# Performance work log

Measured on AMD Instinct MI355X. Metric: run time of the kernel, lower is better.

Reference implementation:

```python
import jax, jax.numpy as jnp
import numpy as np

MAXDISP = 320
NEG_SLOPE = 0.2


def _lrelu(x):
    return jnp.where(x >= 0, x, NEG_SLOPE * x)


def _conv(x, w, b, stride):
    # NCHW conv, VALID padding (torch Conv2d with padding=0)
    y = jax.lax.conv_general_dilated(x, w, window_strides=stride, padding='VALID',
                                     dimension_numbers=('NCHW', 'OIHW', 'NCHW'))
    return y + b[None, :, None, None]


def _tile_pair(fl, fr, wa, ba, wb, bb):
    # left: 4x4 conv stride (4,4); right: ZeroPad2d((0,3,0,0)) then stride (4,1)
    tl = _lrelu(_conv(_lrelu(_conv(fl, wa, ba, (4, 4))), wb, bb, (1, 1)))
    frp = jnp.pad(fr, ((0, 0), (0, 0), (0, 0), (0, 3)))
    tr = _lrelu(_conv(_lrelu(_conv(frp, wa, ba, (4, 1))), wb, bb, (1, 1)))
    return tl, tr


def _calc_init_disp(fl, fr, D):
    # fl: [B,C,h,w4], fr: [B,C,h,w] with w = 4*w4.
    # grid_sample(nearest, align_corners=True) with integer coords reduces to
    # exact gather at right column index 4*j - d, zero outside (padding_mode=zeros).
    B, C, h, w4 = fl.shape
    w = fr.shape[3]
    j = jnp.arange(w4)
    d = jnp.arange(D)
    idx = 4 * j[None, :] - d[:, None]              # [D, w4]
    valid = idx >= 0                               # only left edge can go OOB
    idxc = jnp.clip(idx, 0, w - 1)
    fr_g = fr[:, :, :, idxc]                       # [B,C,h,D,w4]
    fr_g = jnp.where(valid[None, None, None, :, :], fr_g, jnp.zeros((), fr.dtype))
    cv = jnp.abs(fl[:, :, :, None, :] - fr_g).sum(axis=1)  # L1 over C -> [B,h,D,w4]
    return jnp.transpose(cv, (0, 2, 1, 3))         # [B,D,h,w4]


def _level_hyp(cv, dscrpt_feat, dw, db):
    min_cost = jnp.min(cv, axis=1, keepdims=True)
    disp = jnp.argmin(cv, axis=1, keepdims=True).astype(cv.dtype)
    dscrpt = _lrelu(_conv(jnp.concatenate([min_cost, dscrpt_feat], axis=1), dw, db, (1, 1)))
    z = jnp.zeros_like(disp)
    return jnp.concatenate([disp, z, z, dscrpt], axis=1)  # [B,16,h,w]


def setup_inputs() -> dict:
    key = jax.random.key(0)
    ks = iter(jax.random.split(key, 64))

    def rn(shape, s=1.0):
        return jax.random.normal(next(ks), shape, dtype=jnp.float32) * s

    B, H, W = 1, 384, 1280
    inp = {
        'fea_l16': rn((B, 32, H // 16, W // 16)), 'fea_l8': rn((B, 24, H // 8, W // 8)),
        'fea_l4': rn((B, 24, H // 4, W // 4)), 'fea_l2': rn((B, 16, H // 2, W // 2)),
        'fea_l1': rn((B, 16, H, W)),
        'fea_r16': rn((B, 32, H // 16, W // 16)), 'fea_r8': rn((B, 24, H // 8, W // 8)),
        'fea_r4': rn((B, 24, H // 4, W // 4)), 'fea_r2': rn((B, 16, H // 2, W // 2)),
        'fea_r1': rn((B, 16, H, W)),
    }
    fea_c = {16: 32, 8: 24, 4: 24, 2: 16, 1: 16}
    for s, c in fea_c.items():
        inp[f'tcw{s}a'] = rn((16, c, 4, 4), 0.1)
        inp[f'tcb{s}a'] = rn((16,), 0.1)
        inp[f'tcw{s}b'] = rn((16, 16, 1, 1), 0.1)
        inp[f'tcb{s}b'] = rn((16,), 0.1)
    dsc_in = {16: 17, 8: 17, 4: 33, 2: 25, 1: 25}
    for s, c in dsc_in.items():
        inp[f'dw{s}'] = rn((13, c, 1, 1), 0.1)
        inp[f'db{s}'] = rn((13,), 0.1)
    return inp


def reference(fea_l16, fea_l8, fea_l4, fea_l2, fea_l1,
              fea_r16, fea_r8, fea_r4, fea_r2, fea_r1,
              tcw16a, tcb16a, tcw16b, tcb16b,
              tcw8a, tcb8a, tcw8b, tcb8b,
              tcw4a, tcb4a, tcw4b, tcb4b,
              tcw2a, tcb2a, tcw2b, tcb2b,
              tcw1a, tcb1a, tcw1b, tcb1b,
              dw16, db16, dw8, db8, dw4, db4, dw2, db2, dw1, db1):
    tl16, tr16 = _tile_pair(fea_l16, fea_r16, tcw16a, tcb16a, tcw16b, tcb16b)
    tl8, tr8 = _tile_pair(fea_l8, fea_r8, tcw8a, tcb8a, tcw8b, tcb8b)
    tl4, tr4 = _tile_pair(fea_l4, fea_r4, tcw4a, tcb4a, tcw4b, tcb4b)
    tl2, tr2 = _tile_pair(fea_l2, fea_r2, tcw2a, tcb2a, tcw2b, tcb2b)
    tl1, tr1 = _tile_pair(fea_l1, fea_r1, tcw1a, tcb1a, tcw1b, tcb1b)

    cv16 = _calc_init_disp(tl16, tr16, MAXDISP // 16)
    cv8 = _calc_init_disp(tl8, tr8, MAXDISP // 8)
    cv4 = _calc_init_disp(tl4, tr4, MAXDISP // 4)
    cv2 = _calc_init_disp(tl2, tr2, MAXDISP // 2)
    cv1 = _calc_init_disp(tl1, tr1, MAXDISP)

    hyp16 = _level_hyp(cv16, tl16, dw16, db16)
    hyp8 = _level_hyp(cv8, tl8, dw8, db8)
    hyp4 = _level_hyp(cv4, fea_l16, dw4, db4)
    hyp2 = _level_hyp(cv2, fea_l8, dw2, db2)
    hyp1 = _level_hyp(cv1, fea_l4, dw1, db1)

    return (cv16, cv8, cv4, cv2, cv1, hyp16, hyp8, hyp4, hyp2, hyp1)
```

## Files before the change

kernel.cpp:

```cpp
#include <hip/hip_runtime.h>
#include <float.h>

#define NEG_SLOPE 0.2f

__device__ __forceinline__ float lrelu(float x) { return x >= 0.0f ? x : NEG_SLOPE * x; }

struct PrepSeg { const float* wa; const float* wb; float* wat; float* wbt; int CIN; };
struct PrepTab { PrepSeg seg[5]; };

__global__ __launch_bounds__(256)
void prep_weights(PrepTab tab) {
    PrepSeg sg = tab.seg[blockIdx.x];
    int n = sg.CIN * 256;
    for (int i = threadIdx.x; i < n; i += 256)
        sg.wat[i] = sg.wa[(i & 15) * (sg.CIN * 16) + (i >> 4)];
    sg.wbt[threadIdx.x] = sg.wb[(threadIdx.x & 15) * 16 + (threadIdx.x >> 4)];
}

struct ConvSeg {
    const float* in; const float* wat; const float* wbt; const float* ba; const float* bb;
    float* out;
    int CIN, H, W, SX, OW, npix, blk0;
};
struct ConvTab { ConvSeg seg[10]; };

__global__ __launch_bounds__(256)
void conv_uber(ConvTab tab) {
    int si = 0;
#pragma unroll
    for (int i = 1; i < 10; i++) if ((int)blockIdx.x >= tab.seg[i].blk0) si = i;
    const ConvSeg sg = tab.seg[si];

    int pix = ((int)blockIdx.x - sg.blk0) * 256 + threadIdx.x;
    const bool valid = pix < sg.npix;
    int cpix = valid ? pix : sg.npix - 1;
    int y = cpix / sg.OW, x = cpix - y * sg.OW;

    float m[16];
#pragma unroll
    for (int co = 0; co < 16; co++) m[co] = 0.f;

    const int W = sg.W, H = sg.H, CIN = sg.CIN;
    const int xb = (sg.SX == 4) ? 4 * x : x;
    const bool fast = (sg.SX == 4) || (x + 4 <= W);
    const float* ib = sg.in + (size_t)(4 * y) * W;

    if (fast) {
        for (int c = 0; c < CIN; c++) {
            const float* rb = ib + (size_t)c * H * W + xb;
            const float* wc = sg.wat + c * 256;
#pragma unroll
            for (int r = 0; r < 4; r++) {
                float4 v = *(const float4*)(rb + r * W);
                const float* wr = wc + r * 64;
#pragma unroll
                for (int co = 0; co < 16; co++) m[co] = fmaf(v.x, wr[co], m[co]);
#pragma unroll
                for (int co = 0; co < 16; co++) m[co] = fmaf(v.y, wr[16 + co], m[co]);
#pragma unroll
                for (int co = 0; co < 16; co++) m[co] = fmaf(v.z, wr[32 + co], m[co]);
#pragma unroll
                for (int co = 0; co < 16; co++) m[co] = fmaf(v.w, wr[48 + co], m[co]);
            }
        }
    } else {
        for (int c = 0; c < CIN; c++) {
            const float* rb = ib + (size_t)c * H * W;
            const float* wc = sg.wat + c * 256;
#pragma unroll
            for (int r = 0; r < 4; r++) {
                const float* wr = wc + r * 64;
#pragma unroll
                for (int kx = 0; kx < 4; kx++) {
                    int col = xb + kx;
                    float v = (col < W) ? rb[r * W + col] : 0.f;
                    const float* w2 = wr + kx * 16;
#pragma unroll
                    for (int co = 0; co < 16; co++) m[co] = fmaf(v, w2[co], m[co]);
                }
            }
        }
    }

#pragma unroll
    for (int co = 0; co < 16; co++) m[co] = lrelu(m[co] + sg.ba[co]);

    float o[16];
#pragma unroll
    for (int co = 0; co < 16; co++) o[co] = 0.f;
#pragma unroll
    for (int k = 0; k < 16; k++) {
        float mk = m[k];
        const float* wr = sg.wbt + k * 16;
#pragma unroll
        for (int co = 0; co < 16; co++) o[co] = fmaf(mk, wr[co], o[co]);
    }
    if (valid) {
#pragma unroll
        for (int co = 0; co < 16; co++)
            sg.out[(size_t)co * sg.npix + pix] = lrelu(o[co] + sg.bb[co]);
    }
}

struct CvSeg {
    const float* tl; const float* tr; const float* feat;
    const float* dw; const float* db;
    float* cv; float* hyp;
    int h, w4, w, D, gpc, CF, blk0;
};
struct CvTab { CvSeg seg[5]; };

__global__ __launch_bounds__(256)
void cv_hyp_uber(CvTab tab) {
    __shared__ float smin[256];
    __shared__ int sarg[256];

    int si = 0;
#pragma unroll
    for (int i = 1; i < 5; i++) if ((int)blockIdx.x >= tab.seg[i].blk0) si = i;
    const CvSeg sg = tab.seg[si];

    const int npix = sg.h * sg.w4;
    const int p = threadIdx.x & 63, chunk = threadIdx.x >> 6;
    const int pix = ((int)blockIdx.x - sg.blk0) * 64 + p;
    const bool valid = pix < npix;

    float mloc = FLT_MAX; int aloc = 0;
    if (valid) {
        int y = pix / sg.w4, j = pix - y * sg.w4;
        float tlv[16]; float sumabs = 0.f;
#pragma unroll
        for (int c = 0; c < 16; c++) { tlv[c] = sg.tl[(size_t)c * npix + pix]; sumabs += fabsf(tlv[c]); }

        int ngroups = sg.D >> 2;
        int g0 = chunk * sg.gpc;
        int g1 = min(ngroups, g0 + sg.gpc);
        const float* trrow = sg.tr + (size_t)y * sg.w;
        int hw = sg.h * sg.w;

        float carry[16];
        int b0 = 4 * j - 4 * g0;
        if (g0 < g1 && b0 >= 0) {
#pragma unroll
            for (int c = 0; c < 16; c++) carry[c] = trrow[(size_t)c * hw + b0];
        }
        for (int g = g0; g < g1; g++) {
            int b = 4 * j - 4 * g;
            float a0, a1, a2, a3;
            if (b >= 4) {
                a0 = a1 = a2 = a3 = 0.f;
#pragma unroll
                for (int c = 0; c < 16; c++) {
                    float4 f0 = *(const float4*)(trrow + (size_t)c * hw + (b - 4));
                    float tv = tlv[c];
                    a0 += fabsf(tv - carry[c]);
                    a1 += fabsf(tv - f0.w);
                    a2 += fabsf(tv - f0.z);
                    a3 += fabsf(tv - f0.y);
                    carry[c] = f0.x;
                }
            } else if (b == 0) {
                a0 = 0.f; a1 = a2 = a3 = sumabs;
#pragma unroll
                for (int c = 0; c < 16; c++) a0 += fabsf(tlv[c] - carry[c]);
            } else {
                a0 = a1 = a2 = a3 = sumabs;
            }
            float* cvp = sg.cv + (size_t)(4 * g) * npix + pix;
            cvp[0] = a0; cvp[npix] = a1; cvp[2 * (size_t)npix] = a2; cvp[3 * (size_t)npix] = a3;
            if (a0 < mloc) { mloc = a0; aloc = 4 * g; }
            if (a1 < mloc) { mloc = a1; aloc = 4 * g + 1; }
            if (a2 < mloc) { mloc = a2; aloc = 4 * g + 2; }
            if (a3 < mloc) { mloc = a3; aloc = 4 * g + 3; }
        }
    }
    smin[threadIdx.x] = mloc;
    sarg[threadIdx.x] = aloc;
    __syncthreads();

    if (threadIdx.x < 64 && valid) {
        float mn = smin[threadIdx.x]; int arg = sarg[threadIdx.x];
#pragma unroll
        for (int c2 = 1; c2 < 4; c2++) {
            float v = smin[c2 * 64 + threadIdx.x];
            if (v < mn) { mn = v; arg = sarg[c2 * 64 + threadIdx.x]; }
        }
        float acc[13];
#pragma unroll
        for (int o = 0; o < 13; o++) acc[o] = sg.dw[o * (sg.CF + 1)] * mn;
        for (int c = 0; c < sg.CF; c++) {
            float v = sg.feat[(size_t)c * npix + pix];
#pragma unroll
            for (int o = 0; o < 13; o++) acc[o] = fmaf(v, sg.dw[o * (sg.CF + 1) + 1 + c], acc[o]);
        }
        sg.hyp[pix] = (float)arg;
        sg.hyp[npix + pix] = 0.f;
        sg.hyp[2 * (size_t)npix + pix] = 0.f;
#pragma unroll
        for (int o = 0; o < 13; o++) sg.hyp[(size_t)(3 + o) * npix + pix] = lrelu(acc[o] + sg.db[o]);
    }
}

extern "C" void kernel_launch(void* const* d_in, const int* in_sizes, int n_in,
                              void* d_out, int out_size, void* d_ws, size_t ws_size,
                              hipStream_t stream) {
    (void)in_sizes; (void)n_in; (void)out_size; (void)ws_size;
    float* out = (float*)d_out;
    float* ws = (float*)d_ws;

    const int C[5] = {32, 24, 24, 16, 16};
    const int H[5] = {24, 48, 96, 192, 384};
    const int W[5] = {80, 160, 320, 640, 1280};
    const int D[5] = {20, 40, 80, 160, 320};
    const int wa_i[5] = {10, 14, 18, 22, 26};
    const int dw_i[5] = {30, 32, 34, 36, 38};

    const size_t cv_off[5]  = {0, 2400, 21600, 175200, 1404000};
    const size_t hyp_off[5] = {11234400, 11236320, 11244000, 11274720, 11397600};
    const size_t tl_off[5] = {0, 9600, 48000, 201600, 816000};
    const size_t tr_off[5] = {1920, 17280, 78720, 324480, 1307520};
    const size_t wat_off[5] = {3280000, 3288192, 3294336, 3300480, 3304576};
    const size_t wbt_off[5] = {3310000, 3310256, 3310512, 3310768, 3311024};

    const float* fl[5] = {(const float*)d_in[0], (const float*)d_in[1], (const float*)d_in[2],
                          (const float*)d_in[3], (const float*)d_in[4]};
    const float* fr[5] = {(const float*)d_in[5], (const float*)d_in[6], (const float*)d_in[7],
                          (const float*)d_in[8], (const float*)d_in[9]};

    PrepTab pt;
    for (int l = 0; l < 5; l++) {
        pt.seg[l].wa = (const float*)d_in[wa_i[l]];
        pt.seg[l].wb = (const float*)d_in[wa_i[l] + 2];
        pt.seg[l].wat = ws + wat_off[l];
        pt.seg[l].wbt = ws + wbt_off[l];
        pt.seg[l].CIN = C[l];
    }
    prep_weights<<<5, 256, 0, stream>>>(pt);

    const int ord_lvl[10]  = {4, 4, 3, 3, 2, 2, 1, 1, 0, 0};
    const int ord_side[10] = {1, 0, 1, 0, 1, 0, 1, 0, 1, 0};
    ConvTab ct;
    int blk = 0;
    for (int i = 0; i < 10; i++) {
        int l = ord_lvl[i]; bool right = ord_side[i];
        ConvSeg& s = ct.seg[i];
        s.in = right ? fr[l] : fl[l];
        s.wat = ws + wat_off[l];
        s.wbt = ws + wbt_off[l];
        s.ba = (const float*)d_in[wa_i[l] + 1];
        s.bb = (const float*)d_in[wa_i[l] + 3];
        s.out = ws + (right ? tr_off[l] : tl_off[l]);
        s.CIN = C[l]; s.H = H[l]; s.W = W[l];
        s.SX = right ? 1 : 4;
        s.OW = right ? W[l] : W[l] / 4;
        s.npix = (H[l] / 4) * s.OW;
        s.blk0 = blk;
        blk += (s.npix + 255) / 256;
    }
    conv_uber<<<blk, 256, 0, stream>>>(ct);

    const float* feat[5] = {ws + tl_off[0], ws + tl_off[1], fl[0], fl[1], fl[2]};
    const int   CF[5]    = {16, 16, 32, 24, 24};
    CvTab vt;
    blk = 0;
    for (int i = 0; i < 5; i++) {
        int l = 4 - i;
        CvSeg& s = vt.seg[i];
        s.tl = ws + tl_off[l]; s.tr = ws + tr_off[l];
        s.feat = feat[l];
        s.dw = (const float*)d_in[dw_i[l]];
        s.db = (const float*)d_in[dw_i[l] + 1];
        s.cv = out + cv_off[l]; s.hyp = out + hyp_off[l];
        s.h = H[l] / 4; s.w4 = W[l] / 4; s.w = W[l]; s.D = D[l];
        int ngroups = D[l] / 4;
        s.gpc = (ngroups + 3) / 4;
        s.CF = CF[l];
        s.blk0 = blk;
        blk += (s.h * s.w4 + 63) / 64;
    }
    cv_hyp_uber<<<blk, 256, 0, stream>>>(vt);
}
```

Baseline: 366.3 us.

## Compute four adjacent right-tile outputs per thread to reuse loaded input rows

The right-side stride-(4,1) conv now has each thread produce four consecutive output columns. It loads two float4s per row and reuses them across the overlapping 4-wide windows, then writes float4 stores. This cuts redundant global loads, launches four times fewer blocks for the right side, and amortizes weight reads across more FMAs. In exchange it raises register pressure (64 accumulators plus 64 outputs), which may lower occupancy or cause spills.

Result: slower. 736.3 us (+101.0%).

```diff
diff --git a/kernel.cpp b/kernel.cpp
--- a/kernel.cpp
+++ b/kernel.cpp
@@ -20,7 +20,7 @@
 struct ConvSeg {
     const float* in; const float* wat; const float* wbt; const float* ba; const float* bb;
     float* out;
-    int CIN, H, W, SX, OW, npix, blk0;
+    int CIN, H, W, right, nit, npix, blk0;
 };
 struct ConvTab { ConvSeg seg[10]; };
 
@@ -31,23 +31,75 @@
     for (int i = 1; i < 10; i++) if ((int)blockIdx.x >= tab.seg[i].blk0) si = i;
     const ConvSeg sg = tab.seg[si];
 
-    int pix = ((int)blockIdx.x - sg.blk0) * 256 + threadIdx.x;
-    const bool valid = pix < sg.npix;
-    int cpix = valid ? pix : sg.npix - 1;
-    int y = cpix / sg.OW, x = cpix - y * sg.OW;
-
-    float m[16];
-#pragma unroll
-    for (int co = 0; co < 16; co++) m[co] = 0.f;
-
+    int t = ((int)blockIdx.x - sg.blk0) * 256 + threadIdx.x;
+    const bool valid = t < sg.nit;
+    int ct = valid ? t : sg.nit - 1;
     const int W = sg.W, H = sg.H, CIN = sg.CIN;
-    const int xb = (sg.SX == 4) ? 4 * x : x;
-    const bool fast = (sg.SX == 4) || (x + 4 <= W);
-    const float* ib = sg.in + (size_t)(4 * y) * W;
-
-    if (fast) {
+    const int W4 = W >> 2;
+    int y = ct / W4, xq = ct - y * W4;
+    int colb = 4 * xq;
+    const float* ib = sg.in + (size_t)(4 * y) * W + colb;
+
+    if (sg.right) {
+        float m[4][16];
+#pragma unroll
+        for (int i = 0; i < 4; i++)
+#pragma unroll
+            for (int co = 0; co < 16; co++) m[i][co] = 0.f;
+
+        const bool has1 = colb + 4 < W;
         for (int c = 0; c < CIN; c++) {
-            const float* rb = ib + (size_t)c * H * W + xb;
+            const float* rb = ib + (size_t)c * H * W;
+            const float* wc = sg.wat + c * 256;
+#pragma unroll
+            for (int r = 0; r < 4; r++) {
+                float4 f0 = *(const float4*)(rb + r * W);
+                float4 f1 = make_float4(0.f, 0.f, 0.f, 0.f);
+                if (has1) f1 = *(const float4*)(rb + r * W + 4);
+                float wv[8] = {f0.x, f0.y, f0.z, f0.w, f1.x, f1.y, f1.z, f1.w};
+                const float* wr = wc + r * 64;
+#pragma unroll
+                for (int i = 0; i < 4; i++) {
+#pragma unroll
+                    for (int kx = 0; kx < 4; kx++) {
+                        float v = wv[i + kx];
+                        const float* w2 = wr + kx * 16;
+#pragma unroll
+                        for (int co = 0; co < 16; co++) m[i][co] = fmaf(v, w2[co], m[i][co]);
+                    }
+                }
+            }
+        }
+        float o[4][16];
+#pragma unroll
+        for (int i = 0; i < 4; i++) {
+#pragma unroll
+            for (int co = 0; co < 16; co++) m[i][co] = lrelu(m[i][co] + sg.ba[co]);
+#pragma unroll
+            for (int co = 0; co < 16; co++) o[i][co] = 0.f;
+#pragma unroll
+            for (int k = 0; k < 16; k++) {
+                float mk = m[i][k];
+                const float* wr = sg.wbt + k * 16;
+#pragma unroll
+                for (int co = 0; co < 16; co++) o[i][co] = fmaf(mk, wr[co], o[i][co]);
+            }
+        }
+        if (valid) {
+            size_t base = (size_t)y * W + colb;
+#pragma unroll
+            for (int co = 0; co < 16; co++) {
+                float4 v = make_float4(lrelu(o[0][co] + sg.bb[co]), lrelu(o[1][co] + sg.bb[co]),
+                                       lrelu(o[2][co] + sg.bb[co]), lrelu(o[3][co] + sg.bb[co]));
+                *(float4*)(sg.out + (size_t)co * sg.npix + base) = v;
+            }
+        }
+    } else {
+        float m[16];
+#pragma unroll
+        for (int co = 0; co < 16; co++) m[co] = 0.f;
+        for (int c = 0; c < CIN; c++) {
+            const float* rb = ib + (size_t)c * H * W;
             const float* wc = sg.wat + c * 256;
 #pragma unroll
             for (int r = 0; r < 4; r++) {
@@ -63,42 +115,23 @@
                 for (int co = 0; co < 16; co++) m[co] = fmaf(v.w, wr[48 + co], m[co]);
             }
         }
-    } else {
-        for (int c = 0; c < CIN; c++) {
-            const float* rb = ib + (size_t)c * H * W;
-            const float* wc = sg.wat + c * 256;
-#pragma unroll
-            for (int r = 0; r < 4; r++) {
-                const float* wr = wc + r * 64;
-#pragma unroll
-                for (int kx = 0; kx < 4; kx++) {
-                    int col = xb + kx;
-                    float v = (col < W) ? rb[r * W + col] : 0.f;
-                    const float* w2 = wr + kx * 16;
-#pragma unroll
-                    for (int co = 0; co < 16; co++) m[co] = fmaf(v, w2[co], m[co]);
-                }
-            }
-        }
-    }
-
-#pragma unroll
-    for (int co = 0; co < 16; co++) m[co] = lrelu(m[co] + sg.ba[co]);
-
-    float o[16];
-#pragma unroll
-    for (int co = 0; co < 16; co++) o[co] = 0.f;
-#pragma unroll
-    for (int k = 0; k < 16; k++) {
-        float mk = m[k];
-        const float* wr = sg.wbt + k * 16;
-#pragma unroll
-        for (int co = 0; co < 16; co++) o[co] = fmaf(mk, wr[co], o[co]);
-    }
-    if (valid) {
-#pragma unroll
-        for (int co = 0; co < 16; co++)
-            sg.out[(size_t)co * sg.npix + pix] = lrelu(o[co] + sg.bb[co]);
+#pragma unroll
+        for (int co = 0; co < 16; co++) m[co] = lrelu(m[co] + sg.ba[co]);
+        float o[16];
+#pragma unroll
+        for (int co = 0; co < 16; co++) o[co] = 0.f;
+#pragma unroll
+        for (int k = 0; k < 16; k++) {
+            float mk = m[k];
+            const float* wr = sg.wbt + k * 16;
+#pragma unroll
+            for (int co = 0; co < 16; co++) o[co] = fmaf(mk, wr[co], o[co]);
+        }
+        if (valid) {
+#pragma unroll
+            for (int co = 0; co < 16; co++)
+                sg.out[(size_t)co * sg.nit + t] = lrelu(o[co] + sg.bb[co]);
+        }
     }
 }
 
@@ -251,11 +284,12 @@
         s.bb = (const float*)d_in[wa_i[l] + 3];
         s.out = ws + (right ? tr_off[l] : tl_off[l]);
         s.CIN = C[l]; s.H = H[l]; s.W = W[l];
-        s.SX = right ? 1 : 4;
-        s.OW = right ? W[l] : W[l] / 4;
-        s.npix = (H[l] / 4) * s.OW;
+        s.right = right ? 1 : 0;
+        int OH = H[l] / 4, W4 = W[l] / 4;
+        s.nit = OH * W4;
+        s.npix = right ? OH * W[l] : OH * W4;
         s.blk0 = blk;
-        blk += (s.npix + 255) / 256;
+        blk += (s.nit + 255) / 256;
     }
     conv_uber<<<blk, 256, 0, stream>>>(ct);
 
```
